# Kernel optimization log

Measured on AMD Instinct MI355X. Metric: run time of the kernel, lower is better.

Reference implementation:

```python
import jax, jax.numpy as jnp
import numpy as np

NUM_USERS = 50000
NUM_ITEMS = 10000
NUM_SUPPORT = 5
INPUT_DIM = 512
OUTPUT_DIM = 500
NNZ = 400000


def setup_inputs() -> dict:
    key = jax.random.key(0)
    ks = jax.random.split(key, 6)
    x_u = jax.random.normal(ks[0], (NUM_USERS, INPUT_DIM), dtype=jnp.float32)
    x_v = jax.random.normal(ks[1], (NUM_ITEMS, INPUT_DIM), dtype=jnp.float32)
    # random-uniform-like weight init (weight_variable_random_uniform)
    weights_u = jax.random.normal(ks[2], (INPUT_DIM, OUTPUT_DIM), dtype=jnp.float32) * 0.05
    sup_vals = jax.random.uniform(ks[3], (NUM_SUPPORT, NNZ), dtype=jnp.float32)
    sup_rows = jax.random.randint(ks[4], (NUM_SUPPORT, NNZ), 0, NUM_USERS, dtype=jnp.int32)
    sup_cols = jax.random.randint(ks[5], (NUM_SUPPORT, NNZ), 0, NUM_ITEMS, dtype=jnp.int32)
    return {"x_u": x_u, "x_v": x_v, "weights_u": weights_u,
            "sup_vals": sup_vals, "sup_rows": sup_rows, "sup_cols": sup_cols}


def reference(x_u, x_v, weights_u, sup_vals, sup_rows, sup_cols):
    # share_user_item_weights=True -> weights_v is weights_u; dropout=0.0 -> identity.
    hidden = OUTPUT_DIM // NUM_SUPPORT  # 100
    supports_u, supports_v = [], []
    for i in range(NUM_SUPPORT):
        Wi = jax.lax.dynamic_slice_in_dim(weights_u, i * hidden, hidden, axis=1)
        tmp_u = x_u @ Wi  # [num_users, hidden]
        tmp_v = x_v @ Wi  # [num_items, hidden]
        vals = sup_vals[i][:, None]  # [nnz, 1]
        rows, cols = sup_rows[i], sup_cols[i]
        # support_i @ tmp_v  (sparse [U,I] times dense [I,h])
        su = jax.ops.segment_sum(vals * tmp_v[cols], rows, num_segments=NUM_USERS)
        # support_i^T @ tmp_u (sparse [I,U] times dense [U,h])
        sv = jax.ops.segment_sum(vals * tmp_u[rows], cols, num_segments=NUM_ITEMS)
        supports_u.append(su)
        supports_v.append(sv)
    z_u = jnp.concatenate(supports_u, axis=1)  # [num_users, output_dim]
    z_v = jnp.concatenate(supports_v, axis=1)  # [num_items, output_dim]
    return (jax.nn.relu(z_u), jax.nn.relu(z_v))
```

## Files before the change

### kernel.cpp

```cpp
#include <hip/hip_runtime.h>

#define NUM_USERS   50000
#define NUM_ITEMS   10000
#define NUM_SUPPORT 5
#define INPUT_DIM   512
#define OUTPUT_DIM  500
#define NPAD        512
#define HIDDEN      100
#define HPAD        128
#define NNZ         400000
#define NEDGE       (NUM_SUPPORT * NNZ)

#define CH_E        8192
#define NCHUNK      ((NEDGE + CH_E - 1) / CH_E)
#define NB_U        ((NUM_SUPPORT * NUM_USERS + 255) / 256)
#define NKEY_V2     (NUM_SUPPORT * NUM_ITEMS * 4)
#define NB_V2       ((NKEY_V2 + 255) / 256)
#define HISTM_U_SZ  (NB_U * NCHUNK)
#define HISTM_U_ALIGN 239616
#define HISTM_V_SZ  (NB_V2 * NCHUNK)
#define HISTM_TOT   (HISTM_U_ALIGN + HISTM_V_SZ)

typedef unsigned int u32;
typedef unsigned short ushort_t;
typedef __attribute__((ext_vector_type(4))) float f32x4;
typedef __attribute__((ext_vector_type(8))) short bf16x8;

#define GLDS(g, l) __builtin_amdgcn_global_load_lds( \
    (const __attribute__((address_space(1))) unsigned int*)(g), \
    (__attribute__((address_space(3))) unsigned int*)(l), 16, 0, 0)

__device__ inline ushort_t bf16_rne(float f) {
    u32 u = __float_as_uint(f);
    u32 r = (u + 0x7FFFu + ((u >> 16) & 1u)) >> 16;
    return (ushort_t)r;
}
__device__ inline float bf16_lo_f32(u32 w) { return __uint_as_float(w << 16); }
__device__ inline float bf16_hi_f32(u32 w) { return __uint_as_float(w & 0xFFFF0000u); }

__device__ inline u32 rb3(u32 r) {
    return (r >= 12500u ? 1u : 0u) + (r >= 25000u ? 1u : 0u) + (r >= 37500u ? 1u : 0u);
}

__device__ inline int xcd_swizzle(int bid, int nwg) {
    int q = nwg >> 3, rmd = nwg & 7;
    int xcd = bid & 7, idx = bid >> 3;
    int base = (xcd < rmd) ? xcd * (q + 1) : rmd * (q + 1) + (xcd - rmd) * q;
    return base + idx;
}

__global__ __launch_bounds__(256) void cvt_bf16_2(
    const float4* __restrict__ a, const float4* __restrict__ b,
    ushort4* __restrict__ oa, ushort4* __restrict__ ob, int na4, int nb4)
{
    int t = blockIdx.x * 256 + threadIdx.x;
    const float4* src;
    ushort4* dst;
    int idx;
    if (t < na4) { src = a; dst = oa; idx = t; }
    else { idx = t - na4; if (idx >= nb4) return; src = b; dst = ob; }
    float4 v = src[idx];
    ushort4 o;
    o.x = bf16_rne(v.x); o.y = bf16_rne(v.y);
    o.z = bf16_rne(v.z); o.w = bf16_rne(v.w);
    dst[idx] = o;
}

__global__ __launch_bounds__(256) void make_WbT(
    const float* __restrict__ W, ushort_t* __restrict__ WbT)
{
    int t = blockIdx.x * 256 + threadIdx.x;
    int n = t >> 9, k = t & 511;
    float v = (n < OUTPUT_DIM) ? W[k * OUTPUT_DIM + n] : 0.f;
    WbT[t] = bf16_rne(v);
}

#define BM 128
#define BN 128
#define BK 32

__global__ __launch_bounds__(256) void gemm_mfma_bf16(
    const ushort_t* __restrict__ A,
    const ushort_t* __restrict__ BT,
    ushort_t* __restrict__ Xp,
    int M)
{
    const int K = INPUT_DIM;
    __shared__ ushort_t As[BM * BK];
    __shared__ ushort_t Bs[BN * BK];

    const int tid  = threadIdx.x;
    const int wave = tid >> 6;
    const int lane = tid & 63;
    const int quad = lane >> 4;
    const int lr   = lane & 15;
    const int m0 = blockIdx.x * BM;
    const int n0 = blockIdx.y * BN;
    const int wm = (wave >> 1) * 64;
    const int wn = (wave & 1) * 64;

    f32x4 acc[4][4] = {};

    for (int k0 = 0; k0 < K; k0 += BK) {
        #pragma unroll
        for (int h = 0; h < 2; ++h) {
            int o   = tid * 16 + h * 4096;
            int row = o >> 6;
            int byt = o & 63;
            int gr  = m0 + row; if (gr >= M) gr = M - 1;
            GLDS((const char*)A + ((long long)gr * K + k0) * 2 + byt, (char*)As + o);
        }
        #pragma unroll
        for (int h = 0; h < 2; ++h) {
            int o   = tid * 16 + h * 4096;
            int row = o >> 6;
            int byt = o & 63;
            GLDS((const char*)BT + ((long long)(n0 + row) * K + k0) * 2 + byt, (char*)Bs + o);
        }
        asm volatile("s_waitcnt vmcnt(0)" ::: "memory");
        __syncthreads();

        bf16x8 af[4], bfr[4];
        #pragma unroll
        for (int tm = 0; tm < 4; ++tm)
            af[tm] = *(const bf16x8*)(As + (wm + tm * 16 + lr) * BK + quad * 8);
        #pragma unroll
        for (int tn = 0; tn < 4; ++tn)
            bfr[tn] = *(const bf16x8*)(Bs + (wn + tn * 16 + lr) * BK + quad * 8);
        #pragma unroll
        for (int tm = 0; tm < 4; ++tm)
            #pragma unroll
            for (int tn = 0; tn < 4; ++tn)
                acc[tm][tn] = __builtin_amdgcn_mfma_f32_16x16x32_bf16(
                    af[tm], bfr[tn], acc[tm][tn], 0, 0, 0);
        __syncthreads();
    }

    #pragma unroll
    for (int tm = 0; tm < 4; ++tm) {
        int rbase = m0 + wm + tm * 16 + quad * 4;
        #pragma unroll
        for (int tn = 0; tn < 4; ++tn) {
            int col = n0 + wn + tn * 16 + lr;
            if (col >= OUTPUT_DIM) continue;
            int seg = col / HIDDEN;
            int off = col - seg * HIDDEN;
            ushort_t* dst = Xp + (long long)seg * M * HPAD + off;
            #pragma unroll
            for (int g = 0; g < 4; ++g) {
                int row = rbase + g;
                if (row < M) dst[(long long)row * HPAD] = bf16_rne(acc[tm][tn][g]);
            }
        }
    }
}

__global__ __launch_bounds__(256) void scan1(u32* __restrict__ data, int n,
                                             u32* __restrict__ partials)
{
    __shared__ u32 sh[256];
    int t = threadIdx.x;
    int base = blockIdx.x * 1024 + t * 4;
    u32 x[4];
    #pragma unroll
    for (int k = 0; k < 4; ++k) {
        int idx = base + k;
        x[k] = (idx < n) ? data[idx] : 0u;
    }
    u32 tsum = x[0] + x[1] + x[2] + x[3];
    sh[t] = tsum;
    __syncthreads();
    for (int off = 1; off < 256; off <<= 1) {
        u32 v = (t >= off) ? sh[t - off] : 0u;
        __syncthreads();
        sh[t] += v;
        __syncthreads();
    }
    u32 run = (t > 0) ? sh[t - 1] : 0u;
    if (t == 255) partials[blockIdx.x] = sh[255];
    #pragma unroll
    for (int k = 0; k < 4; ++k) {
        int idx = base + k;
        if (idx < n) data[idx] = run;
        run += x[k];
    }
}

__global__ __launch_bounds__(512) void scan_partials(u32* __restrict__ partials, int n)
{
    __shared__ u32 sh[512];
    int t = threadIdx.x;
    u32 x = (t < n) ? partials[t] : 0u;
    sh[t] = x;
    __syncthreads();
    for (int off = 1; off < 512; off <<= 1) {
        u32 v = (t >= off) ? sh[t - off] : 0u;
        __syncthreads();
        sh[t] += v;
        __syncthreads();
    }
    if (t < n) partials[t] = (t > 0) ? sh[t - 1] : 0u;
}

__global__ __launch_bounds__(256) void scan_add(u32* __restrict__ data, int n,
                                                const u32* __restrict__ partials)
{
    int idx = blockIdx.x * 256 + threadIdx.x;
    if (idx >= n) return;
    u32 adj = (idx >= HISTM_U_ALIGN) ? (u32)NEDGE : 0u;
    data[idx] = data[idx] + partials[idx >> 10] - adj;
}

__global__ __launch_bounds__(256) void hist_uv(
    const int* __restrict__ rows, const int* __restrict__ cols,
    u32* __restrict__ histm_u, u32* __restrict__ histm_v)
{
    __shared__ u32 hu[NB_U];
    __shared__ u32 hv[NB_V2];
    const int tid = threadIdx.x;
    const int c = blockIdx.x;
    if (c == 0)
        for (int z = HISTM_U_SZ + tid; z < HISTM_U_ALIGN; z += 256) histm_u[z] = 0u;
    for (int b = tid; b < NB_U; b += 256) hu[b] = 0u;
    for (int b = tid; b < NB_V2; b += 256) hv[b] = 0u;
    __syncthreads();
    int base = c * CH_E;
    int end = base + CH_E; if (end > NEDGE) end = NEDGE;
    for (int e = base + tid; e < end; e += 256) {
        unsigned i = (unsigned)e / (unsigned)NNZ;
        u32 r = (u32)rows[e];
        u32 ku = i * (u32)NUM_USERS + r;
        u32 knew = (i * (u32)NUM_ITEMS + (u32)cols[e]) * 4u + rb3(r);
        atomicAdd(&hu[ku >> 8], 1u);
        atomicAdd(&hv[knew >> 8], 1u);
    }
    __syncthreads();
    for (int b = tid; b < NB_U; b += 256) histm_u[b * NCHUNK + c] = hu[b];
    for (int b = tid; b < NB_V2; b += 256) histm_v[b * NCHUNK + c] = hv[b];
}

__global__ __launch_bounds__(256) void partition_uv(
    const int* __restrict__ rows, const int* __restrict__ cols,
    const float* __restrict__ vals,
    const u32* __restrict__ histm_u, const u32* __restrict__ histm_v,
    uint2* __restrict__ buf_u, uint2* __restrict__ buf_v)
{
    __shared__ u32 cu[NB_U];
    __shared__ u32 cv[NB_V2];
    const int tid = threadIdx.x;
    const int c = blockIdx.x;
    for (int b = tid; b < NB_U; b += 256) cu[b] = histm_u[b * NCHUNK + c];
    for (int b = tid; b < NB_V2; b += 256) cv[b] = histm_v[b * NCHUNK + c];
    __syncthreads();
    int base = c * CH_E;
    int end = base + CH_E; if (end > NEDGE) end = NEDGE;
    for (int e = base + tid; e < end; e += 256) {
        unsigned i = (unsigned)e / (unsigned)NNZ;
        u32 r = (u32)rows[e];
        u32 col = (u32)cols[e];
        u32 vb = __float_as_uint(vals[e]);
        u32 ku = i * (u32)NUM_USERS + r;
        u32 kv16 = i * (u32)NUM_ITEMS + col;
        u32 knew = kv16 * 4u + rb3(r);
        u32 pu = atomicAdd(&cu[ku >> 8], 1u);
        uint2 eu; eu.x = vb; eu.y = (ku << 14) | col;
        buf_u[pu] = eu;
        u32 pv = atomicAdd(&cv[knew >> 8], 1u);
        uint2 ev; ev.x = vb; ev.y = (kv16 << 16) | r;
        buf_v[pv] = ev;
    }
}

__device__ inline void bucket_body_u(
    int b, const uint2* __restrict__ buf, const u32* __restrict__ histm,
    u32* __restrict__ ptr, uint2* __restrict__ perm,
    u32* cnt, u32* scn)
{
    constexpr int NKEY = NUM_SUPPORT * NUM_USERS;
    constexpr int NB = NB_U;
    const int tid = threadIdx.x;
    const u32 key0 = (u32)b << 8;
    const u32 start = histm[b * NCHUNK];
    const u32 bend  = (b + 1 < NB) ? histm[(b + 1) * NCHUNK] : (u32)NEDGE;
    if (b == 0 && tid == 0) ptr[NKEY] = (u32)NEDGE;
    cnt[tid] = 0u;
    __syncthreads();
    for (u32 j = start + tid; j < bend; j += 256) {
        u32 key = buf[j].y >> 14;
        atomicAdd(&cnt[key - key0], 1u);
    }
    __syncthreads();
    scn[tid] = cnt[tid];
    __syncthreads();
    for (int off = 1; off < 256; off <<= 1) {
        u32 v = (tid >= off) ? scn[tid - off] : 0u;
        __syncthreads();
        scn[tid] += v;
        __syncthreads();
    }
    u32 myoff = start + scn[tid] - cnt[tid];
    if (key0 + (u32)tid < (u32)NKEY) ptr[key0 + tid] = myoff;
    __syncthreads();
    cnt[tid] = myoff;
    __syncthreads();
    for (u32 j = start + tid; j < bend; j += 256) {
        uint2 q = buf[j];
        u32 key = q.y >> 14;
        u32 p = atomicAdd(&cnt[key - key0], 1u);
        uint2 out;
        out.x = q.x;
        out.y = q.y & 0x3FFFu;
        perm[p] = out;
    }
}

__device__ inline void bucket_body_v(
    int b, const uint2* __restrict__ buf, const u32* __restrict__ histm,
    u32* __restrict__ ptr, uint2* __restrict__ perm,
    u32* cnt, u32* scn)
{
    constexpr int NKEY = NKEY_V2;
    constexpr int NB = NB_V2;
    const int tid = threadIdx.x;
    const u32 key0 = (u32)b << 8;
    const u32 start = histm[b * NCHUNK];
    const u32 bend  = (b + 1 < NB) ? histm[(b + 1) * NCHUNK] : (u32)NEDGE;
    if (b == 0 && tid == 0) ptr[NKEY] = (u32)NEDGE;
    cnt[tid] = 0u;
    __syncthreads();
    for (u32 j = start + tid; j < bend; j += 256) {
        u32 y = buf[j].y;
        u32 key = (y >> 16) * 4u + rb3(y & 0xFFFFu);
        atomicAdd(&cnt[key - key0], 1u);
    }
    __syncthreads();
    scn[tid] = cnt[tid];
    __syncthreads();
    for (int off = 1; off < 256; off <<= 1) {
        u32 v = (tid >= off) ? scn[tid - off] : 0u;
        __syncthreads();
        scn[tid] += v;
        __syncthreads();
    }
    u32 myoff = start + scn[tid] - cnt[tid];
    if (key0 + (u32)tid < (u32)NKEY) ptr[key0 + tid] = myoff;
    __syncthreads();
    cnt[tid] = myoff;
    __syncthreads();
    for (u32 j = start + tid; j < bend; j += 256) {
        uint2 q = buf[j];
        u32 key = (q.y >> 16) * 4u + rb3(q.y & 0xFFFFu);
        u32 p = atomicAdd(&cnt[key - key0], 1u);
        uint2 out;
        out.x = q.x;
        out.y = q.y & 0xFFFFu;
        perm[p] = out;
    }
}

__global__ __launch_bounds__(256) void bucket_scatter_uv(
    const uint2* __restrict__ buf_u, const u32* __restrict__ histm_u,
    u32* __restrict__ ptr_u, uint2* __restrict__ perm_u,
    const uint2* __restrict__ buf_v, const u32* __restrict__ histm_v,
    u32* __restrict__ ptr_v, uint2* __restrict__ perm_v)
{
    __shared__ u32 cnt[256];
    __shared__ u32 scn[256];
    if (blockIdx.x < NB_U)
        bucket_body_u(blockIdx.x, buf_u, histm_u, ptr_u, perm_u, cnt, scn);
    else
        bucket_body_v(blockIdx.x - NB_U, buf_v, histm_v, ptr_v, perm_v, cnt, scn);
}

template<int NROWS, int PSTR>
__global__ __launch_bounds__(256) void spmm_pack4(
    const u32* __restrict__ ptr,
    const uint2* __restrict__ perm,
    const ushort_t* __restrict__ Xp,
    float* __restrict__ Z,
    int nsrc)
{
    constexpr int NKEY = NUM_SUPPORT * NROWS;
    int bid = xcd_swizzle(blockIdx.x, gridDim.x);
    int w = bid * 4 + (int)(threadIdx.x >> 6);
    w = __builtin_amdgcn_readfirstlane(w);
    if (w * 4 >= NKEY) return;
    const int lane = threadIdx.x & 63;
    const int g  = lane >> 4;
    const int sl = lane & 15;

    int key = w * 4 + g;
    int i = key / NROWS;
    int r = key - i * NROWS;
    u32 s = ptr[key * PSTR];
    u32 e = ptr[(key + 1) * PSTR];

    const ushort_t* Xs = Xp + (long long)i * nsrc * HPAD + sl * 8;

    u32 m = e - s;
    { u32 t = (u32)__shfl_xor((int)m, 16); m = m > t ? m : t; }
    { u32 t = (u32)__shfl_xor((int)m, 32); m = m > t ? m : t; }
    int iters = (int)((m + 3) >> 2);

    float a0 = 0.f, a1 = 0.f, a2 = 0.f, a3 = 0.f;
    float a4 = 0.f, a5 = 0.f, a6 = 0.f, a7 = 0.f;
    u32 k = s;
    for (int it = 0; it < iters; ++it) {
        bool p0 = k < e, p1 = (k + 1) < e, p2 = (k + 2) < e, p3 = (k + 3) < e;
        u32 j0 = p0 ? k : 0u;
        u32 j1 = p1 ? (k + 1) : 0u;
        u32 j2 = p2 ? (k + 2) : 0u;
        u32 j3 = p3 ? (k + 3) : 0u;
        uint2 q0 = perm[j0], q1 = perm[j1], q2 = perm[j2], q3 = perm[j3];
        float v0 = p0 ? __uint_as_float(q0.x) : 0.f;
        float v1 = p1 ? __uint_as_float(q1.x) : 0.f;
        float v2 = p2 ? __uint_as_float(q2.x) : 0.f;
        float v3 = p3 ? __uint_as_float(q3.x) : 0.f;
        uint4 w0 = *(const uint4*)(Xs + ((long long)q0.y << 7));
        uint4 w1 = *(const uint4*)(Xs + ((long long)q1.y << 7));
        uint4 w2 = *(const uint4*)(Xs + ((long long)q2.y << 7));
        uint4 w3 = *(const uint4*)(Xs + ((long long)q3.y << 7));
        a0 += v0 * bf16_lo_f32(w0.x) + v1 * bf16_lo_f32(w1.x)
            + v2 * bf16_lo_f32(w2.x) + v3 * bf16_lo_f32(w3.x);
        a1 += v0 * bf16_hi_f32(w0.x) + v1 * bf16_hi_f32(w1.x)
            + v2 * bf16_hi_f32(w2.x) + v3 * bf16_hi_f32(w3.x);
        a2 += v0 * bf16_lo_f32(w0.y) + v1 * bf16_lo_f32(w1.y)
            + v2 * bf16_lo_f32(w2.y) + v3 * bf16_lo_f32(w3.y);
        a3 += v0 * bf16_hi_f32(w0.y) + v1 * bf16_hi_f32(w1.y)
            + v2 * bf16_hi_f32(w2.y) + v3 * bf16_hi_f32(w3.y);
        a4 += v0 * bf16_lo_f32(w0.z) + v1 * bf16_lo_f32(w1.z)
            + v2 * bf16_lo_f32(w2.z) + v3 * bf16_lo_f32(w3.z);
        a5 += v0 * bf16_hi_f32(w0.z) + v1 * bf16_hi_f32(w1.z)
            + v2 * bf16_hi_f32(w2.z) + v3 * bf16_hi_f32(w3.z);
        a6 += v0 * bf16_lo_f32(w0.w) + v1 * bf16_lo_f32(w1.w)
            + v2 * bf16_lo_f32(w2.w) + v3 * bf16_lo_f32(w3.w);
        a7 += v0 * bf16_hi_f32(w0.w) + v1 * bf16_hi_f32(w1.w)
            + v2 * bf16_hi_f32(w2.w) + v3 * bf16_hi_f32(w3.w);
        k += 4;
    }

    if (sl < 13) {
        float* zp = Z + (long long)r * OUTPUT_DIM + i * HIDDEN + sl * 8;
        float4 o0;
        o0.x = a0 > 0.f ? a0 : 0.f;
        o0.y = a1 > 0.f ? a1 : 0.f;
        o0.z = a2 > 0.f ? a2 : 0.f;
        o0.w = a3 > 0.f ? a3 : 0.f;
        *(float4*)zp = o0;
        if (sl < 12) {
            float4 o1;
            o1.x = a4 > 0.f ? a4 : 0.f;
            o1.y = a5 > 0.f ? a5 : 0.f;
            o1.z = a6 > 0.f ? a6 : 0.f;
            o1.w = a7 > 0.f ? a7 : 0.f;
            *(float4*)(zp + 4) = o1;
        }
    }
}

#define TM 64
#define TN 64
#define TK 16

__global__ __launch_bounds__(256) void gemm_f32(
    const float* __restrict__ A, const float* __restrict__ B,
    float* __restrict__ C, int M, int N, int K, int ldc)
{
    __shared__ float Asl[TK][TM + 4];
    __shared__ float Bsl[TK][TN + 4];
    const int tid = threadIdx.x;
    const int tx  = tid & 15;
    const int ty  = tid >> 4;
    const int row0 = blockIdx.x * TM;
    const int col0 = blockIdx.y * TN;
    float acc[4][4] = {};
    for (int k0 = 0; k0 < K; k0 += TK) {
        #pragma unroll
        for (int it = 0; it < (TM * TK) / 256; ++it) {
            int idx = tid + it * 256;
            int m = idx >> 4, kk = idx & 15, gr = row0 + m;
            Asl[kk][m] = (gr < M) ? A[(long long)gr * K + (k0 + kk)] : 0.f;
        }
        #pragma unroll
        for (int it = 0; it < (TK * TN) / 256; ++it) {
            int idx = tid + it * 256;
            int kk = idx >> 6, n = idx & 63, gc = col0 + n;
            Bsl[kk][n] = (gc < N) ? B[(long long)(k0 + kk) * N + gc] : 0.f;
        }
        __syncthreads();
        #pragma unroll
        for (int kk = 0; kk < TK; ++kk) {
            float a[4], b[4];
            #pragma unroll
            for (int u = 0; u < 4; ++u) a[u] = Asl[kk][ty * 4 + u];
            #pragma unroll
            for (int v = 0; v < 4; ++v) b[v] = Bsl[kk][tx * 4 + v];
            #pragma unroll
            for (int u = 0; u < 4; ++u)
                #pragma unroll
                for (int v = 0; v < 4; ++v)
                    acc[u][v] += a[u] * b[v];
        }
        __syncthreads();
    }
    #pragma unroll
    for (int u = 0; u < 4; ++u) {
        int gr = row0 + ty * 4 + u;
        if (gr >= M) continue;
        #pragma unroll
        for (int v = 0; v < 4; ++v) {
            int gc = col0 + tx * 4 + v;
            if (gc < N) C[(long long)gr * ldc + gc] = acc[u][v];
        }
    }
}

__global__ __launch_bounds__(256) void scatter_edges(
    const float* __restrict__ sup_vals,
    const int*   __restrict__ sup_rows,
    const int*   __restrict__ sup_cols,
    const float* __restrict__ XU, const float* __restrict__ XV,
    float* __restrict__ z_u, float* __restrict__ z_v)
{
    const unsigned t = blockIdx.x * 256u + threadIdx.x;
    const unsigned total = (unsigned)NEDGE * HIDDEN;
    if (t >= total) return;
    const unsigned j  = t % HIDDEN;
    const unsigned eg = t / HIDDEN;
    const unsigned i  = eg / NNZ;
    const float val = sup_vals[eg];
    const int   r   = sup_rows[eg];
    const int   c   = sup_cols[eg];
    const int   colOff = i * HIDDEN + j;
    atomicAdd(&z_u[(long long)r * OUTPUT_DIM + colOff],
              val * XV[(long long)c * NPAD + colOff]);
    atomicAdd(&z_v[(long long)c * OUTPUT_DIM + colOff],
              val * XU[(long long)r * NPAD + colOff]);
}

__global__ __launch_bounds__(256) void relu_inplace(float4* __restrict__ p, int n4)
{
    int t = blockIdx.x * 256 + threadIdx.x;
    if (t >= n4) return;
    float4 v = p[t];
    v.x = v.x > 0.f ? v.x : 0.f;
    v.y = v.y > 0.f ? v.y : 0.f;
    v.z = v.z > 0.f ? v.z : 0.f;
    v.w = v.w > 0.f ? v.w : 0.f;
    p[t] = v;
}

extern "C" void kernel_launch(void* const* d_in, const int* in_sizes, int n_in,
                              void* d_out, int out_size, void* d_ws, size_t ws_size,
                              hipStream_t stream)
{
    const float* x_u      = (const float*)d_in[0];
    const float* x_v      = (const float*)d_in[1];
    const float* W        = (const float*)d_in[2];
    const float* sup_vals = (const float*)d_in[3];
    const int*   sup_rows = (const int*)d_in[4];
    const int*   sup_cols = (const int*)d_in[5];

    float* z_u = (float*)d_out;
    float* z_v = z_u + (long long)NUM_USERS * OUTPUT_DIM;

    const long long NU = (long long)NUM_USERS * 512;
    const long long NV = (long long)NUM_ITEMS * 512;
    const long long PU = (long long)NUM_SUPPORT * NUM_USERS * HPAD;
    const long long PV = (long long)NUM_SUPPORT * NUM_ITEMS * HPAD;
    const int NRU = NUM_SUPPORT * NUM_USERS;
    const int NRV = NUM_SUPPORT * NUM_ITEMS;

    ushort_t* Xp_u  = (ushort_t*)d_ws;
    ushort_t* Xp_v  = Xp_u + PU;
    ushort_t* xu_in = Xp_v + PV;
    ushort_t* xv_in = xu_in + NU;
    ushort_t* WbT   = xv_in + NV;
    u32* row_ptr_u  = (u32*)(WbT + 512 * 512);
    u32* col_ptr_v  = row_ptr_u + (NRU + 1);
    u32* partials   = col_ptr_v + (NKEY_V2 + 1);
    size_t need_full = ((char*)(partials + 512)) - ((char*)d_ws);

    uint2* buf_v    = (uint2*)xu_in;
    u32*   histm_u  = (u32*)(buf_v + NEDGE);
    u32*   histm_v  = histm_u + HISTM_U_ALIGN;
    uint2* perm_u   = (uint2*)(histm_v + HISTM_V_SZ);
    uint2* perm_v   = perm_u + NEDGE;
    uint2* buf_u    = (uint2*)z_u;

    dim3 blk(256);

    if (ws_size >= need_full) {
        {
            int na4 = (int)(NU / 4), nb4 = (int)(NV / 4);
            cvt_bf16_2<<<(na4 + nb4 + 255) / 256, blk, 0, stream>>>(
                (const float4*)x_u, (const float4*)x_v,
                (ushort4*)xu_in, (ushort4*)xv_in, na4, nb4);
        }
        make_WbT<<<(512 * 512) / 256, blk, 0, stream>>>(W, WbT);
        gemm_mfma_bf16<<<dim3((NUM_USERS + BM - 1) / BM, 512 / BN), blk, 0, stream>>>(
            xu_in, WbT, Xp_u, NUM_USERS);
        gemm_mfma_bf16<<<dim3((NUM_ITEMS + BM - 1) / BM, 512 / BN), blk, 0, stream>>>(
            xv_in, WbT, Xp_v, NUM_ITEMS);

        hist_uv<<<NCHUNK, blk, 0, stream>>>(sup_rows, sup_cols, histm_u, histm_v);

        {
            int nb = (HISTM_TOT + 1023) / 1024;
            scan1<<<nb, blk, 0, stream>>>(histm_u, HISTM_TOT, partials);
            scan_partials<<<1, dim3(512), 0, stream>>>(partials, nb);
            scan_add<<<(HISTM_TOT + 255) / 256, blk, 0, stream>>>(
                histm_u, HISTM_TOT, partials);
        }

        partition_uv<<<NCHUNK, blk, 0, stream>>>(
            sup_rows, sup_cols, sup_vals, histm_u, histm_v, buf_u, buf_v);

        bucket_scatter_uv<<<NB_U + NB_V2, blk, 0, stream>>>(
            buf_u, histm_u, row_ptr_u, perm_u,
            buf_v, histm_v, col_ptr_v, perm_v);

        spmm_pack4<NUM_USERS, 1><<<((NRU / 4) * 64) / 256, blk, 0, stream>>>(
            row_ptr_u, perm_u, Xp_v, z_u, NUM_ITEMS);
        spmm_pack4<NUM_ITEMS, 4><<<((NRV / 4) * 64) / 256, blk, 0, stream>>>(
            col_ptr_v, perm_v, Xp_u, z_v, NUM_USERS);
    } else {
        float* XU = (float*)d_ws;
        float* XV = XU + (long long)NUM_USERS * NPAD;
        gemm_f32<<<dim3((NUM_USERS + TM - 1) / TM, (OUTPUT_DIM + TN - 1) / TN),
                   blk, 0, stream>>>(x_u, W, XU, NUM_USERS, OUTPUT_DIM, INPUT_DIM, NPAD);
        gemm_f32<<<dim3((NUM_ITEMS + TM - 1) / TM, (OUTPUT_DIM + TN - 1) / TN),
                   blk, 0, stream>>>(x_v, W, XV, NUM_ITEMS, OUTPUT_DIM, INPUT_DIM, NPAD);
        hipMemsetAsync(d_out, 0, (size_t)out_size * sizeof(float), stream);
        unsigned total = (unsigned)NEDGE * HIDDEN;
        scatter_edges<<<(total + 255u) / 256u, blk, 0, stream>>>(
            sup_vals, sup_rows, sup_cols, XU, XV, z_u, z_v);
        int n4 = out_size / 4;
        relu_inplace<<<(n4 + 255) / 256, blk, 0, stream>>>((float4*)d_out, n4);
    }
}
```

Before: 513.7 us.

## Fuse conversion and SpMM launches, reorder v-side key layout and GEMM grid

Merges the bf16 conversion of x_u/x_v with the W transpose into a single kernel and merges the two SpMM kernels into one launch, removing launch gaps and letting the user and item sides share the GPU. The v-side sort key changes from (support,item,row-band) to (support,row-band,item), so the v-side SpMM walks four row-band segments per item with stride-1 pointer reads instead of a strided pointer array. The GEMM grid is transposed so consecutive blocks share the same A row tile. In exchange, bucket_body_v now recovers the support index with an integer divide per edge, and the spmm loop runs four separate segment loops, each padded to a multiple of four edges.

New measurement: 509.0 us. No clear change (-0.9%).

```diff
diff --git a/kernel.cpp b/kernel.cpp
--- a/kernel.cpp
+++ b/kernel.cpp
@@ -14,7 +14,7 @@
 #define CH_E        8192
 #define NCHUNK      ((NEDGE + CH_E - 1) / CH_E)
 #define NB_U        ((NUM_SUPPORT * NUM_USERS + 255) / 256)
-#define NKEY_V2     (NUM_SUPPORT * NUM_ITEMS * 4)
+#define NKEY_V2     (NUM_SUPPORT * 4 * NUM_ITEMS)
 #define NB_V2       ((NKEY_V2 + 255) / 256)
 #define HISTM_U_SZ  (NB_U * NCHUNK)
 #define HISTM_U_ALIGN 239616
@@ -41,6 +41,9 @@
 __device__ inline u32 rb3(u32 r) {
     return (r >= 12500u ? 1u : 0u) + (r >= 25000u ? 1u : 0u) + (r >= 37500u ? 1u : 0u);
 }
+__device__ inline u32 vkey(u32 i, u32 col, u32 r) {
+    return (i * 4u + rb3(r)) * (u32)NUM_ITEMS + col;
+}
 
 __device__ inline int xcd_swizzle(int bid, int nwg) {
     int q = nwg >> 3, rmd = nwg & 7;
@@ -49,30 +52,36 @@
     return base + idx;
 }
 
-__global__ __launch_bounds__(256) void cvt_bf16_2(
+__global__ __launch_bounds__(256) void cvt_all(
     const float4* __restrict__ a, const float4* __restrict__ b,
-    ushort4* __restrict__ oa, ushort4* __restrict__ ob, int na4, int nb4)
+    const float* __restrict__ W,
+    ushort4* __restrict__ oa, ushort4* __restrict__ ob,
+    ushort_t* __restrict__ WbT, int na4, int nb4)
 {
     int t = blockIdx.x * 256 + threadIdx.x;
-    const float4* src;
-    ushort4* dst;
-    int idx;
-    if (t < na4) { src = a; dst = oa; idx = t; }
-    else { idx = t - na4; if (idx >= nb4) return; src = b; dst = ob; }
-    float4 v = src[idx];
-    ushort4 o;
-    o.x = bf16_rne(v.x); o.y = bf16_rne(v.y);
-    o.z = bf16_rne(v.z); o.w = bf16_rne(v.w);
-    dst[idx] = o;
-}
-
-__global__ __launch_bounds__(256) void make_WbT(
-    const float* __restrict__ W, ushort_t* __restrict__ WbT)
-{
-    int t = blockIdx.x * 256 + threadIdx.x;
-    int n = t >> 9, k = t & 511;
-    float v = (n < OUTPUT_DIM) ? W[k * OUTPUT_DIM + n] : 0.f;
-    WbT[t] = bf16_rne(v);
+    if (t < na4) {
+        float4 v = a[t];
+        ushort4 o;
+        o.x = bf16_rne(v.x); o.y = bf16_rne(v.y);
+        o.z = bf16_rne(v.z); o.w = bf16_rne(v.w);
+        oa[t] = o;
+        return;
+    }
+    int t2 = t - na4;
+    if (t2 < nb4) {
+        float4 v = b[t2];
+        ushort4 o;
+        o.x = bf16_rne(v.x); o.y = bf16_rne(v.y);
+        o.z = bf16_rne(v.z); o.w = bf16_rne(v.w);
+        ob[t2] = o;
+        return;
+    }
+    int t3 = t2 - nb4;
+    if (t3 < 512 * 512) {
+        int n = t3 >> 9, k = t3 & 511;
+        float v = (n < OUTPUT_DIM) ? W[k * OUTPUT_DIM + n] : 0.f;
+        WbT[t3] = bf16_rne(v);
+    }
 }
 
 #define BM 128
@@ -94,8 +103,8 @@
     const int lane = tid & 63;
     const int quad = lane >> 4;
     const int lr   = lane & 15;
-    const int m0 = blockIdx.x * BM;
-    const int n0 = blockIdx.y * BN;
+    const int m0 = blockIdx.y * BM;
+    const int n0 = blockIdx.x * BN;
     const int wm = (wave >> 1) * 64;
     const int wn = (wave & 1) * 64;
 
@@ -230,7 +239,7 @@
         unsigned i = (unsigned)e / (unsigned)NNZ;
         u32 r = (u32)rows[e];
         u32 ku = i * (u32)NUM_USERS + r;
-        u32 knew = (i * (u32)NUM_ITEMS + (u32)cols[e]) * 4u + rb3(r);
+        u32 knew = vkey(i, (u32)cols[e], r);
         atomicAdd(&hu[ku >> 8], 1u);
         atomicAdd(&hv[knew >> 8], 1u);
     }
@@ -261,7 +270,7 @@
         u32 vb = __float_as_uint(vals[e]);
         u32 ku = i * (u32)NUM_USERS + r;
         u32 kv16 = i * (u32)NUM_ITEMS + col;
-        u32 knew = kv16 * 4u + rb3(r);
+        u32 knew = vkey(i, col, r);
         u32 pu = atomicAdd(&cu[ku >> 8], 1u);
         uint2 eu; eu.x = vb; eu.y = (ku << 14) | col;
         buf_u[pu] = eu;
@@ -330,7 +339,10 @@
     __syncthreads();
     for (u32 j = start + tid; j < bend; j += 256) {
         u32 y = buf[j].y;
-        u32 key = (y >> 16) * 4u + rb3(y & 0xFFFFu);
+        u32 kv16 = y >> 16;
+        u32 i = kv16 / (u32)NUM_ITEMS;
+        u32 col = kv16 - i * (u32)NUM_ITEMS;
+        u32 key = vkey(i, col, y & 0xFFFFu);
         atomicAdd(&cnt[key - key0], 1u);
     }
     __syncthreads();
@@ -349,7 +361,10 @@
     __syncthreads();
     for (u32 j = start + tid; j < bend; j += 256) {
         uint2 q = buf[j];
-        u32 key = (q.y >> 16) * 4u + rb3(q.y & 0xFFFFu);
+        u32 kv16 = q.y >> 16;
+        u32 i = kv16 / (u32)NUM_ITEMS;
+        u32 col = kv16 - i * (u32)NUM_ITEMS;
+        u32 key = vkey(i, col, q.y & 0xFFFFu);
         u32 p = atomicAdd(&cnt[key - key0], 1u);
         uint2 out;
         out.x = q.x;
@@ -372,75 +387,78 @@
         bucket_body_v(blockIdx.x - NB_U, buf_v, histm_v, ptr_v, perm_v, cnt, scn);
 }
 
-template<int NROWS, int PSTR>
-__global__ __launch_bounds__(256) void spmm_pack4(
+template<int NROWS, int RBN>
+__device__ inline void spmm_body(
+    int bid, int nwg,
     const u32* __restrict__ ptr,
     const uint2* __restrict__ perm,
     const ushort_t* __restrict__ Xp,
     float* __restrict__ Z,
     int nsrc)
 {
-    constexpr int NKEY = NUM_SUPPORT * NROWS;
-    int bid = xcd_swizzle(blockIdx.x, gridDim.x);
+    bid = xcd_swizzle(bid, nwg);
     int w = bid * 4 + (int)(threadIdx.x >> 6);
     w = __builtin_amdgcn_readfirstlane(w);
-    if (w * 4 >= NKEY) return;
     const int lane = threadIdx.x & 63;
     const int g  = lane >> 4;
     const int sl = lane & 15;
 
     int key = w * 4 + g;
     int i = key / NROWS;
-    int r = key - i * NROWS;
-    u32 s = ptr[key * PSTR];
-    u32 e = ptr[(key + 1) * PSTR];
+    int c = key - i * NROWS;
 
     const ushort_t* Xs = Xp + (long long)i * nsrc * HPAD + sl * 8;
-
-    u32 m = e - s;
-    { u32 t = (u32)__shfl_xor((int)m, 16); m = m > t ? m : t; }
-    { u32 t = (u32)__shfl_xor((int)m, 32); m = m > t ? m : t; }
-    int iters = (int)((m + 3) >> 2);
 
     float a0 = 0.f, a1 = 0.f, a2 = 0.f, a3 = 0.f;
     float a4 = 0.f, a5 = 0.f, a6 = 0.f, a7 = 0.f;
-    u32 k = s;
-    for (int it = 0; it < iters; ++it) {
-        bool p0 = k < e, p1 = (k + 1) < e, p2 = (k + 2) < e, p3 = (k + 3) < e;
-        u32 j0 = p0 ? k : 0u;
-        u32 j1 = p1 ? (k + 1) : 0u;
-        u32 j2 = p2 ? (k + 2) : 0u;
-        u32 j3 = p3 ? (k + 3) : 0u;
-        uint2 q0 = perm[j0], q1 = perm[j1], q2 = perm[j2], q3 = perm[j3];
-        float v0 = p0 ? __uint_as_float(q0.x) : 0.f;
-        float v1 = p1 ? __uint_as_float(q1.x) : 0.f;
-        float v2 = p2 ? __uint_as_float(q2.x) : 0.f;
-        float v3 = p3 ? __uint_as_float(q3.x) : 0.f;
-        uint4 w0 = *(const uint4*)(Xs + ((long long)q0.y << 7));
-        uint4 w1 = *(const uint4*)(Xs + ((long long)q1.y << 7));
-        uint4 w2 = *(const uint4*)(Xs + ((long long)q2.y << 7));
-        uint4 w3 = *(const uint4*)(Xs + ((long long)q3.y << 7));
-        a0 += v0 * bf16_lo_f32(w0.x) + v1 * bf16_lo_f32(w1.x)
-            + v2 * bf16_lo_f32(w2.x) + v3 * bf16_lo_f32(w3.x);
-        a1 += v0 * bf16_hi_f32(w0.x) + v1 * bf16_hi_f32(w1.x)
-            + v2 * bf16_hi_f32(w2.x) + v3 * bf16_hi_f32(w3.x);
-        a2 += v0 * bf16_lo_f32(w0.y) + v1 * bf16_lo_f32(w1.y)
-            + v2 * bf16_lo_f32(w2.y) + v3 * bf16_lo_f32(w3.y);
-        a3 += v0 * bf16_hi_f32(w0.y) + v1 * bf16_hi_f32(w1.y)
-            + v2 * bf16_hi_f32(w2.y) + v3 * bf16_hi_f32(w3.y);
-        a4 += v0 * bf16_lo_f32(w0.z) + v1 * bf16_lo_f32(w1.z)
-            + v2 * bf16_lo_f32(w2.z) + v3 * bf16_lo_f32(w3.z);
-        a5 += v0 * bf16_hi_f32(w0.z) + v1 * bf16_hi_f32(w1.z)
-            + v2 * bf16_hi_f32(w2.z) + v3 * bf16_hi_f32(w3.z);
-        a6 += v0 * bf16_lo_f32(w0.w) + v1 * bf16_lo_f32(w1.w)
-            + v2 * bf16_lo_f32(w2.w) + v3 * bf16_lo_f32(w3.w);
-        a7 += v0 * bf16_hi_f32(w0.w) + v1 * bf16_hi_f32(w1.w)
-            + v2 * bf16_hi_f32(w2.w) + v3 * bf16_hi_f32(w3.w);
-        k += 4;
+
+    #pragma unroll
+    for (int rb = 0; rb < RBN; ++rb) {
+        int kk = (i * RBN + rb) * NROWS + c;
+        u32 s = ptr[kk];
+        u32 e = ptr[kk + 1];
+        u32 m = e - s;
+        { u32 t = (u32)__shfl_xor((int)m, 16); m = m > t ? m : t; }
+        { u32 t = (u32)__shfl_xor((int)m, 32); m = m > t ? m : t; }
+        int iters = (int)((m + 3) >> 2);
+        u32 k = s;
+        for (int it = 0; it < iters; ++it) {
+            bool p0 = k < e, p1 = (k + 1) < e, p2 = (k + 2) < e, p3 = (k + 3) < e;
+            u32 j0 = p0 ? k : 0u;
+            u32 j1 = p1 ? (k + 1) : 0u;
+            u32 j2 = p2 ? (k + 2) : 0u;
+            u32 j3 = p3 ? (k + 3) : 0u;
+            uint2 q0 = perm[j0], q1 = perm[j1], q2 = perm[j2], q3 = perm[j3];
+            float v0 = p0 ? __uint_as_float(q0.x) : 0.f;
+            float v1 = p1 ? __uint_as_float(q1.x) : 0.f;
+            float v2 = p2 ? __uint_as_float(q2.x) : 0.f;
+            float v3 = p3 ? __uint_as_float(q3.x) : 0.f;
+            uint4 w0 = *(const uint4*)(Xs + ((long long)q0.y << 7));
+            uint4 w1 = *(const uint4*)(Xs + ((long long)q1.y << 7));
+            uint4 w2 = *(const uint4*)(Xs + ((long long)q2.y << 7));
+            uint4 w3 = *(const uint4*)(Xs + ((long long)q3.y << 7));
+            a0 += v0 * bf16_lo_f32(w0.x) + v1 * bf16_lo_f32(w1.x)
+                + v2 * bf16_lo_f32(w2.x) + v3 * bf16_lo_f32(w3.x);
+            a1 += v0 * bf16_hi_f32(w0.x) + v1 * bf16_hi_f32(w1.x)
+                + v2 * bf16_hi_f32(w2.x) + v3 * bf16_hi_f32(w3.x);
+            a2 += v0 * bf16_lo_f32(w0.y) + v1 * bf16_lo_f32(w1.y)
+                + v2 * bf16_lo_f32(w2.y) + v3 * bf16_lo_f32(w3.y);
+            a3 += v0 * bf16_hi_f32(w0.y) + v1 * bf16_hi_f32(w1.y)
+                + v2 * bf16_hi_f32(w2.y) + v3 * bf16_hi_f32(w3.y);
+            a4 += v0 * bf16_lo_f32(w0.z) + v1 * bf16_lo_f32(w1.z)
+                + v2 * bf16_lo_f32(w2.z) + v3 * bf16_lo_f32(w3.z);
+            a5 += v0 * bf16_hi_f32(w0.z) + v1 * bf16_hi_f32(w1.z)
+                + v2 * bf16_hi_f32(w2.z) + v3 * bf16_hi_f32(w3.z);
+            a6 += v0 * bf16_lo_f32(w0.w) + v1 * bf16_lo_f32(w1.w)
+                + v2 * bf16_lo_f32(w2.w) + v3 * bf16_lo_f32(w3.w);
+            a7 += v0 * bf16_hi_f32(w0.w) + v1 * bf16_hi_f32(w1.w)
+                + v2 * bf16_hi_f32(w2.w) + v3 * bf16_hi_f32(w3.w);
+            k += 4;
+        }
     }
 
     if (sl < 13) {
-        float* zp = Z + (long long)r * OUTPUT_DIM + i * HIDDEN + sl * 8;
+        float* zp = Z + (long long)c * OUTPUT_DIM + i * HIDDEN + sl * 8;
         float4 o0;
         o0.x = a0 > 0.f ? a0 : 0.f;
         o0.y = a1 > 0.f ? a1 : 0.f;
@@ -456,6 +474,21 @@
             *(float4*)(zp + 4) = o1;
         }
     }
+}
+
+#define NBU4 ((NUM_SUPPORT * NUM_USERS) / 16)
+#define NBV4 ((NUM_SUPPORT * NUM_ITEMS) / 16)
+
+__global__ __launch_bounds__(256) void spmm_both(
+    const u32* __restrict__ ptr_u, const uint2* __restrict__ perm_u,
+    const ushort_t* __restrict__ Xp_v, float* __restrict__ z_u,
+    const u32* __restrict__ ptr_v, const uint2* __restrict__ perm_v,
+    const ushort_t* __restrict__ Xp_u, float* __restrict__ z_v)
+{
+    if ((int)blockIdx.x < NBU4)
+        spmm_body<NUM_USERS, 1>(blockIdx.x, NBU4, ptr_u, perm_u, Xp_v, z_u, NUM_ITEMS);
+    else
+        spmm_body<NUM_ITEMS, 4>(blockIdx.x - NBU4, NBV4, ptr_v, perm_v, Xp_u, z_v, NUM_USERS);
 }
 
 #define TM 64
@@ -593,14 +626,14 @@
     if (ws_size >= need_full) {
         {
             int na4 = (int)(NU / 4), nb4 = (int)(NV / 4);
-            cvt_bf16_2<<<(na4 + nb4 + 255) / 256, blk, 0, stream>>>(
-                (const float4*)x_u, (const float4*)x_v,
-                (ushort4*)xu_in, (ushort4*)xv_in, na4, nb4);
-        }
-        make_WbT<<<(512 * 512) / 256, blk, 0, stream>>>(W, WbT);
-        gemm_mfma_bf16<<<dim3((NUM_USERS + BM - 1) / BM, 512 / BN), blk, 0, stream>>>(
+            int tot = na4 + nb4 + 512 * 512;
+            cvt_all<<<(tot + 255) / 256, blk, 0, stream>>>(
+                (const float4*)x_u, (const float4*)x_v, W,
+                (ushort4*)xu_in, (ushort4*)xv_in, WbT, na4, nb4);
+        }
+        gemm_mfma_bf16<<<dim3(512 / BN, (NUM_USERS + BM - 1) / BM), blk, 0, stream>>>(
             xu_in, WbT, Xp_u, NUM_USERS);
-        gemm_mfma_bf16<<<dim3((NUM_ITEMS + BM - 1) / BM, 512 / BN), blk, 0, stream>>>(
+        gemm_mfma_bf16<<<dim3(512 / BN, (NUM_ITEMS + BM - 1) / BM), blk, 0, stream>>>(
             xv_in, WbT, Xp_v, NUM_ITEMS);
 
         hist_uv<<<NCHUNK, blk, 0, stream>>>(sup_rows, sup_cols, histm_u, histm_v);
@@ -620,10 +653,9 @@
             buf_u, histm_u, row_ptr_u, perm_u,
             buf_v, histm_v, col_ptr_v, perm_v);
 
-        spmm_pack4<NUM_USERS, 1><<<((NRU / 4) * 64) / 256, blk, 0, stream>>>(
-            row_ptr_u, perm_u, Xp_v, z_u, NUM_ITEMS);
-        spmm_pack4<NUM_ITEMS, 4><<<((NRV / 4) * 64) / 256, blk, 0, stream>>>(
-            col_ptr_v, perm_v, Xp_u, z_v, NUM_USERS);
+        spmm_both<<<NBU4 + NBV4, blk, 0, stream>>>(
+            row_ptr_u, perm_u, Xp_v, z_u,
+            col_ptr_v, perm_v, Xp_u, z_v);
     } else {
         float* XU = (float*)d_ws;
         float* XV = XU + (long long)NUM_USERS * NPAD;
```
